# Kernel optimization log

Hardware: AMD Instinct MI355X
Metric: run time of the kernel (lower is better)

The kernel has to match this reference:

```python
import jax, jax.numpy as jnp
import numpy as np

SCORE_THRESHOLD = 0.15
IOU_THRESHOLD = 0.5
MAX_OUTPUT = 10          # tf.image.non_max_suppression(..., 10, ...)
NUM_CLASSES = 80
NUM_ANCHORS = 5
NEG = -1e9               # score for suppressed / below-threshold boxes


def setup_inputs() -> dict:
    key = jax.random.key(0)
    k1, k2 = jax.random.split(key)
    preds = jax.random.normal(k1, (16, 52, 52, NUM_ANCHORS * (5 + NUM_CLASSES)), dtype=jnp.float32)
    # anchor priors in grid-cell units, typical YOLOv2 range
    anchors = jax.random.uniform(k2, (NUM_ANCHORS, 2), dtype=jnp.float32, minval=0.5, maxval=6.0)
    return {"preds": preds, "anchors": anchors}


def _decode(preds, anchors):
    """YOLOv2 head decode (the `_interpret_prediction` callable)."""
    B, H, W, _ = preds.shape
    A = anchors.shape[0]
    p = preds.reshape(B, H, W, A, 5 + NUM_CLASSES)
    gy, gx = jnp.meshgrid(jnp.arange(H, dtype=preds.dtype),
                          jnp.arange(W, dtype=preds.dtype), indexing="ij")
    grid = jnp.stack([gx, gy], axis=-1)[None, :, :, None, :]   # (1,H,W,1,2) in (x,y)
    dims = jnp.array([W, H], dtype=preds.dtype)
    box_xy = (jax.nn.sigmoid(p[..., :2]) + grid) / dims        # normalized centers
    box_wh = jnp.exp(p[..., 2:4]) * anchors[None, None, None, :, :] / dims
    box_confidence = jax.nn.sigmoid(p[..., 4:5])
    box_class_probs = jax.nn.softmax(p[..., 5:], axis=-1)
    return box_xy, box_wh, box_confidence, box_class_probs


def _iou(box, boxes):
    """IoU of one box (ymin,xmin,ymax,xmax) against all boxes [N,4]."""
    tl = jnp.maximum(box[:2], boxes[:, :2])
    br = jnp.minimum(box[2:], boxes[:, 2:])
    inter = jnp.prod(jnp.maximum(br - tl, 0.0), axis=-1)
    area1 = jnp.prod(jnp.maximum(box[2:] - box[:2], 0.0))
    area2 = jnp.prod(jnp.maximum(boxes[:, 2:] - boxes[:, :2], 0.0), axis=-1)
    return inter / (area1 + area2 - inter + 1e-9)


def reference(preds, anchors):
    box_xy, box_wh, box_confidence, box_class_probs = _decode(preds, anchors)
    box_mins = box_xy - box_wh / 2.0
    box_maxes = box_xy + box_wh / 2.0
    # (ymin, xmin, ymax, xmax), matching the K.concatenate in the source
    boxes = jnp.concatenate([box_mins[..., 1:2], box_mins[..., 0:1],
                             box_maxes[..., 1:2], box_maxes[..., 0:1]], axis=-1)
    box_scores = box_confidence * box_class_probs
    box_classes = jnp.argmax(box_scores, axis=-1)
    box_class_scores = jnp.max(box_scores, axis=-1)

    boxes = boxes.reshape(-1, 4)                       # [N,4]
    scores = box_class_scores.reshape(-1)              # [N]
    classes = box_classes.reshape(-1).astype(preds.dtype)

    # score-threshold mask: instead of boolean_mask (dynamic shape), kill scores
    live = jnp.where(scores >= SCORE_THRESHOLD, scores, NEG)

    # greedy NMS, fixed MAX_OUTPUT iterations (semantics of tf.image.non_max_suppression)
    def step(cur_scores, _):
        i = jnp.argmax(cur_scores)
        s = cur_scores[i]
        valid = s > NEG / 2
        box = boxes[i]
        ious = _iou(box, boxes)
        nxt = jnp.where(ious > IOU_THRESHOLD, NEG, cur_scores).at[i].set(NEG)
        row = jnp.where(valid,
                        jnp.concatenate([box, s[None], classes[i][None]]),
                        jnp.zeros((6,), dtype=preds.dtype))
        return nxt, row

    _, rows = jax.lax.scan(step, live, None, length=MAX_OUTPUT)
    return rows  # [10, 6] = (ymin, xmin, ymax, xmax, score, class); zero rows = padding
```

## Files before the change

### kernel.cpp

```cpp
#include <hip/hip_runtime.h>
#include <math.h>

#define A_N      5
#define GRID_HW  52
#define NCLS     80
#define CH       85
#define SCORE_T  0.15f
#define IOU_T    0.5f
#define NEGV     (-1e9f)
#define MAXOUT   10

#define BPB          64
#define DEC_THREADS  256
#define TILE_FLOATS  (BPB * CH)
#define TILE_F4      (TILE_FLOATS / 4)

#define NMS_THREADS  1024
#define NMS_LBOX     8192
#define KA           (NMS_LBOX / NMS_THREADS)

__global__ __launch_bounds__(DEC_THREADS) void decode_kernel(
    const float* __restrict__ preds,
    const float* __restrict__ anchors,
    float4* __restrict__ pbox, float* __restrict__ pscore,
    float* __restrict__ pcls,
    int* __restrict__ counter, int N, int capacity)
{
    __shared__ __align__(16) float lds[TILE_FLOATS];

    const int tile = blockIdx.x;
    const long long tile_f4_base = (long long)tile * TILE_F4;
    const long long total_f4 = ((long long)N * CH) / 4;
    const float4* src = (const float4*)preds;
    float4* dst = (float4*)lds;

#pragma unroll
    for (int k = 0; k < (TILE_F4 + DEC_THREADS - 1) / DEC_THREADS; ++k) {
        int idx = (int)threadIdx.x + k * DEC_THREADS;
        if (idx < TILE_F4 && (tile_f4_base + idx) < total_f4)
            dst[idx] = src[tile_f4_base + idx];
    }
    __syncthreads();

    const int b = (int)threadIdx.x >> 2;
    const int q = (int)threadIdx.x & 3;
    const int gi = tile * BPB + b;
    const float* bp = lds + b * CH;
    const float* cl = bp + 5 + q * 20;

    float m = cl[0];
    int   am = q * 20;
#pragma unroll
    for (int j = 1; j < 20; ++j) {
        float x = cl[j];
        if (x > m) { m = x; am = q * 20 + j; }
    }
    float s = 0.0f;
#pragma unroll
    for (int j = 0; j < 20; ++j) s += expf(cl[j] - m);

#pragma unroll
    for (int off = 1; off <= 2; off <<= 1) {
        float m2 = __shfl_xor(m, off);
        float s2 = __shfl_xor(s, off);
        int   am2 = __shfl_xor(am, off);
        float M = fmaxf(m, m2);
        s = s * expf(m - M) + s2 * expf(m2 - M);
        if (m2 > m || (m2 == m && am2 < am)) am = am2;
        m = M;
    }

    if (q == 0 && gi < N) {
        float conf  = 1.0f / (1.0f + expf(-bp[4]));
        float score = conf / s;
        if (score >= SCORE_T) {
            int a = gi % A_N;
            int t = gi / A_N;
            int w = t % GRID_HW;
            int h = (t / GRID_HW) % GRID_HW;
            const float inv = 1.0f / (float)GRID_HW;
            float cx = (1.0f / (1.0f + expf(-bp[0])) + (float)w) * inv;
            float cy = (1.0f / (1.0f + expf(-bp[1])) + (float)h) * inv;
            float bw = expf(bp[2]) * anchors[2 * a]     * inv;
            float bh = expf(bp[3]) * anchors[2 * a + 1] * inv;

            int pos = atomicAdd(counter, 1);
            if (pos < capacity) {
                pbox[pos]   = make_float4(cy - 0.5f * bh, cx - 0.5f * bw,
                                          cy + 0.5f * bh, cx + 0.5f * bw);
                pscore[pos] = score;
                pcls[pos]   = (float)am;
            }
        }
    }
}

__global__ __launch_bounds__(NMS_THREADS) void nms_kernel(
    const float4* __restrict__ pbox, float* __restrict__ pscore,
    const float* __restrict__ pcls, const int* __restrict__ counter,
    int capacity, float* __restrict__ out)
{
    __shared__ __align__(16) float4 lbox[NMS_LBOX];
    __shared__ float psc[16];
    __shared__ int   pix[16];
    __shared__ int   swi;

    int M = *counter;
    if (M > capacity) M = capacity;
    const int tid  = (int)threadIdx.x;
    const int lane = tid & 63;
    const int wid  = tid >> 6;

    if (M <= NMS_LBOX) {
        float sc[KA];
#pragma unroll
        for (int k = 0; k < KA; ++k) {
            int j = tid + (k << 10);
            sc[k] = (j < M) ? pscore[j] : -INFINITY;
            if (j < M) lbox[j] = pbox[j];
        }
        __syncthreads();

        for (int it = 0; it < MAXOUT; ++it) {
            float bs = -INFINITY; int bi = -1;
#pragma unroll
            for (int k = 0; k < KA; ++k) {
                if (sc[k] > bs) { bs = sc[k]; bi = tid + (k << 10); }
            }
#pragma unroll
            for (int off = 32; off; off >>= 1) {
                float os = __shfl_xor(bs, off);
                int   oi = __shfl_xor(bi, off);
                if (os > bs || (os == bs && oi != -1 && (bi == -1 || oi < bi))) {
                    bs = os; bi = oi;
                }
            }
            if (lane == 0) { psc[wid] = bs; pix[wid] = bi; }
            __syncthreads();

            if (wid == 0 && lane < 16) {
                bs = psc[lane]; bi = pix[lane];
#pragma unroll
                for (int off = 8; off; off >>= 1) {
                    float os = __shfl_xor(bs, off);
                    int   oi = __shfl_xor(bi, off);
                    if (os > bs || (os == bs && oi != -1 && (bi == -1 || oi < bi))) {
                        bs = os; bi = oi;
                    }
                }
                if (lane == 0) {
                    bool valid = (bi >= 0) && (bs > NEGV * 0.5f);
                    swi = valid ? bi : -1;
                    if (valid) {
                        float4 b = lbox[bi];
                        out[it*6+0] = b.x; out[it*6+1] = b.y;
                        out[it*6+2] = b.z; out[it*6+3] = b.w;
                        out[it*6+4] = bs;  out[it*6+5] = pcls[bi];
                    } else {
                        out[it*6+0] = 0.f; out[it*6+1] = 0.f; out[it*6+2] = 0.f;
                        out[it*6+3] = 0.f; out[it*6+4] = 0.f; out[it*6+5] = 0.f;
                    }
                }
            }
            __syncthreads();

            int wi = swi;
            if (wi >= 0) {
                float4 wb = lbox[wi];
                float a1 = fmaxf(wb.z - wb.x, 0.f) * fmaxf(wb.w - wb.y, 0.f);
#pragma unroll
                for (int k = 0; k < KA; ++k) {
                    int j = tid + (k << 10);
                    if (j == wi) sc[k] = NEGV;
                    if (j < M) {
                        float4 bj = lbox[j];
                        float ty = fmaxf(wb.x, bj.x);
                        float tx = fmaxf(wb.y, bj.y);
                        float by = fminf(wb.z, bj.z);
                        float bx = fminf(wb.w, bj.w);
                        float inter = fmaxf(by - ty, 0.f) * fmaxf(bx - tx, 0.f);
                        float a2 = fmaxf(bj.z - bj.x, 0.f) * fmaxf(bj.w - bj.y, 0.f);
                        float iou = inter / (a1 + a2 - inter + 1e-9f);
                        if (iou > IOU_T) sc[k] = NEGV;
                    }
                }
            }
        }
    } else {
        for (int it = 0; it < MAXOUT; ++it) {
            float bs = -INFINITY; int bi = -1;
            for (int j = tid; j < M; j += NMS_THREADS) {
                float s = pscore[j];
                if (s > bs) { bs = s; bi = j; }
            }
#pragma unroll
            for (int off = 32; off; off >>= 1) {
                float os = __shfl_xor(bs, off);
                int   oi = __shfl_xor(bi, off);
                if (os > bs || (os == bs && oi != -1 && (bi == -1 || oi < bi))) {
                    bs = os; bi = oi;
                }
            }
            if (lane == 0) { psc[wid] = bs; pix[wid] = bi; }
            __syncthreads();
            if (wid == 0 && lane < 16) {
                bs = psc[lane]; bi = pix[lane];
#pragma unroll
                for (int off = 8; off; off >>= 1) {
                    float os = __shfl_xor(bs, off);
                    int   oi = __shfl_xor(bi, off);
                    if (os > bs || (os == bs && oi != -1 && (bi == -1 || oi < bi))) {
                        bs = os; bi = oi;
                    }
                }
                if (lane == 0) {
                    bool valid = (bi >= 0) && (bs > NEGV * 0.5f);
                    swi = valid ? bi : -1;
                    if (valid) {
                        float4 b = pbox[bi];
                        out[it*6+0] = b.x; out[it*6+1] = b.y;
                        out[it*6+2] = b.z; out[it*6+3] = b.w;
                        out[it*6+4] = bs;  out[it*6+5] = pcls[bi];
                        pscore[bi] = NEGV;
                    } else {
                        out[it*6+0] = 0.f; out[it*6+1] = 0.f; out[it*6+2] = 0.f;
                        out[it*6+3] = 0.f; out[it*6+4] = 0.f; out[it*6+5] = 0.f;
                    }
                }
            }
            __syncthreads();
            int wi = swi;
            if (wi >= 0) {
                float4 wb = pbox[wi];
                float a1 = fmaxf(wb.z - wb.x, 0.f) * fmaxf(wb.w - wb.y, 0.f);
                for (int j = tid; j < M; j += NMS_THREADS) {
                    float4 bj = pbox[j];
                    float ty = fmaxf(wb.x, bj.x);
                    float tx = fmaxf(wb.y, bj.y);
                    float by = fminf(wb.z, bj.z);
                    float bx = fminf(wb.w, bj.w);
                    float inter = fmaxf(by - ty, 0.f) * fmaxf(bx - tx, 0.f);
                    float a2 = fmaxf(bj.z - bj.x, 0.f) * fmaxf(bj.w - bj.y, 0.f);
                    float iou = inter / (a1 + a2 - inter + 1e-9f);
                    if (iou > IOU_T) pscore[j] = NEGV;
                }
            }
            __syncthreads();
        }
    }
}

extern "C" void kernel_launch(void* const* d_in, const int* in_sizes, int n_in,
                              void* d_out, int out_size, void* d_ws, size_t ws_size,
                              hipStream_t stream) {
    (void)n_in; (void)out_size;
    const float* preds   = (const float*)d_in[0];
    const float* anchors = (const float*)d_in[1];
    float* out = (float*)d_out;

    int N = in_sizes[0] / CH;

    char* ws = (char*)d_ws;
    int* counter = (int*)ws;
    size_t avail = (ws_size > 64) ? (ws_size - 64) : 0;
    long long cap = (long long)(avail / (sizeof(float4) + 2 * sizeof(float)));
    if (cap > N) cap = N;
    if (cap < 0) cap = 0;
    int capacity = (int)cap;

    float4* pbox  = (float4*)(ws + 64);
    float* pscore = (float*)(pbox + capacity);
    float* pcls   = pscore + capacity;

    hipMemsetAsync(counter, 0, sizeof(int), stream);

    int nTiles = (N + BPB - 1) / BPB;
    decode_kernel<<<nTiles, DEC_THREADS, 0, stream>>>(
        preds, anchors, pbox, pscore, pcls, counter, N, capacity);
    nms_kernel<<<1, NMS_THREADS, 0, stream>>>(
        pbox, pscore, pcls, counter, capacity, out);
}
```

Baseline: 66.89 us.

## Keep NMS candidate boxes in registers and use fast exp in decode

The NMS kernel no longer stages all candidate boxes in a 128 KB shared array. Each thread keeps its boxes in registers, and the winning box is broadcast through a small shared slot. A barrier is added at the end of each iteration to protect that slot. The decode kernel caches each thread's 20 class logits in registers and swaps expf for the faster, less accurate __expf intrinsic. Register pressure rises with 8 float4 plus 8 scores per thread at 1024 threads, which may cause spills.

```diff
diff --git a/kernel.cpp b/kernel.cpp
--- a/kernel.cpp
+++ b/kernel.cpp
@@ -16,8 +16,10 @@
 #define TILE_F4      (TILE_FLOATS / 4)
 
 #define NMS_THREADS  1024
-#define NMS_LBOX     8192
-#define KA           (NMS_LBOX / NMS_THREADS)
+#define NMS_RCAP     8192
+#define KA           (NMS_RCAP / NMS_THREADS)
+
+__device__ __forceinline__ float fexp(float x) { return __expf(x); }
 
 __global__ __launch_bounds__(DEC_THREADS) void decode_kernel(
     const float* __restrict__ preds,
@@ -48,16 +50,19 @@
     const float* bp = lds + b * CH;
     const float* cl = bp + 5 + q * 20;
 
-    float m = cl[0];
+    float r[20];
+#pragma unroll
+    for (int j = 0; j < 20; ++j) r[j] = cl[j];
+
+    float m = r[0];
     int   am = q * 20;
 #pragma unroll
     for (int j = 1; j < 20; ++j) {
-        float x = cl[j];
-        if (x > m) { m = x; am = q * 20 + j; }
+        if (r[j] > m) { m = r[j]; am = q * 20 + j; }
     }
     float s = 0.0f;
 #pragma unroll
-    for (int j = 0; j < 20; ++j) s += expf(cl[j] - m);
+    for (int j = 0; j < 20; ++j) s += fexp(r[j] - m);
 
 #pragma unroll
     for (int off = 1; off <= 2; off <<= 1) {
@@ -65,13 +70,13 @@
         float s2 = __shfl_xor(s, off);
         int   am2 = __shfl_xor(am, off);
         float M = fmaxf(m, m2);
-        s = s * expf(m - M) + s2 * expf(m2 - M);
+        s = s * fexp(m - M) + s2 * fexp(m2 - M);
         if (m2 > m || (m2 == m && am2 < am)) am = am2;
         m = M;
     }
 
     if (q == 0 && gi < N) {
-        float conf  = 1.0f / (1.0f + expf(-bp[4]));
+        float conf  = 1.0f / (1.0f + fexp(-bp[4]));
         float score = conf / s;
         if (score >= SCORE_T) {
             int a = gi % A_N;
@@ -79,10 +84,10 @@
             int w = t % GRID_HW;
             int h = (t / GRID_HW) % GRID_HW;
             const float inv = 1.0f / (float)GRID_HW;
-            float cx = (1.0f / (1.0f + expf(-bp[0])) + (float)w) * inv;
-            float cy = (1.0f / (1.0f + expf(-bp[1])) + (float)h) * inv;
-            float bw = expf(bp[2]) * anchors[2 * a]     * inv;
-            float bh = expf(bp[3]) * anchors[2 * a + 1] * inv;
+            float cx = (1.0f / (1.0f + fexp(-bp[0])) + (float)w) * inv;
+            float cy = (1.0f / (1.0f + fexp(-bp[1])) + (float)h) * inv;
+            float bw = fexp(bp[2]) * anchors[2 * a]     * inv;
+            float bh = fexp(bp[3]) * anchors[2 * a + 1] * inv;
 
             int pos = atomicAdd(counter, 1);
             if (pos < capacity) {
@@ -100,10 +105,10 @@
     const float* __restrict__ pcls, const int* __restrict__ counter,
     int capacity, float* __restrict__ out)
 {
-    __shared__ __align__(16) float4 lbox[NMS_LBOX];
     __shared__ float psc[16];
     __shared__ int   pix[16];
     __shared__ int   swi;
+    __shared__ float swb[4];
 
     int M = *counter;
     if (M > capacity) M = capacity;
@@ -111,15 +116,15 @@
     const int lane = tid & 63;
     const int wid  = tid >> 6;
 
-    if (M <= NMS_LBOX) {
-        float sc[KA];
+    if (M <= NMS_RCAP) {
+        float4 rb[KA];
+        float  sc[KA];
 #pragma unroll
         for (int k = 0; k < KA; ++k) {
             int j = tid + (k << 10);
-            sc[k] = (j < M) ? pscore[j] : -INFINITY;
-            if (j < M) lbox[j] = pbox[j];
-        }
-        __syncthreads();
+            if (j < M) { sc[k] = pscore[j]; rb[k] = pbox[j]; }
+            else       { sc[k] = -INFINITY; rb[k] = make_float4(0.f,0.f,0.f,0.f); }
+        }
 
         for (int it = 0; it < MAXOUT; ++it) {
             float bs = -INFINITY; int bi = -1;
@@ -152,7 +157,8 @@
                     bool valid = (bi >= 0) && (bs > NEGV * 0.5f);
                     swi = valid ? bi : -1;
                     if (valid) {
-                        float4 b = lbox[bi];
+                        float4 b = pbox[bi];
+                        swb[0] = b.x; swb[1] = b.y; swb[2] = b.z; swb[3] = b.w;
                         out[it*6+0] = b.x; out[it*6+1] = b.y;
                         out[it*6+2] = b.z; out[it*6+3] = b.w;
                         out[it*6+4] = bs;  out[it*6+5] = pcls[bi];
@@ -166,25 +172,23 @@
 
             int wi = swi;
             if (wi >= 0) {
-                float4 wb = lbox[wi];
-                float a1 = fmaxf(wb.z - wb.x, 0.f) * fmaxf(wb.w - wb.y, 0.f);
+                float wy0 = swb[0], wx0 = swb[1], wy1 = swb[2], wx1 = swb[3];
+                float a1 = fmaxf(wy1 - wy0, 0.f) * fmaxf(wx1 - wx0, 0.f);
 #pragma unroll
                 for (int k = 0; k < KA; ++k) {
                     int j = tid + (k << 10);
                     if (j == wi) sc[k] = NEGV;
-                    if (j < M) {
-                        float4 bj = lbox[j];
-                        float ty = fmaxf(wb.x, bj.x);
-                        float tx = fmaxf(wb.y, bj.y);
-                        float by = fminf(wb.z, bj.z);
-                        float bx = fminf(wb.w, bj.w);
-                        float inter = fmaxf(by - ty, 0.f) * fmaxf(bx - tx, 0.f);
-                        float a2 = fmaxf(bj.z - bj.x, 0.f) * fmaxf(bj.w - bj.y, 0.f);
-                        float iou = inter / (a1 + a2 - inter + 1e-9f);
-                        if (iou > IOU_T) sc[k] = NEGV;
-                    }
-                }
-            }
+                    float ty = fmaxf(wy0, rb[k].x);
+                    float tx = fmaxf(wx0, rb[k].y);
+                    float by = fminf(wy1, rb[k].z);
+                    float bx = fminf(wx1, rb[k].w);
+                    float inter = fmaxf(by - ty, 0.f) * fmaxf(bx - tx, 0.f);
+                    float a2 = fmaxf(rb[k].z - rb[k].x, 0.f) * fmaxf(rb[k].w - rb[k].y, 0.f);
+                    float iou = inter / (a1 + a2 - inter + 1e-9f);
+                    if (iou > IOU_T) sc[k] = NEGV;
+                }
+            }
+            __syncthreads();
         }
     } else {
         for (int it = 0; it < MAXOUT; ++it) {
@@ -218,6 +222,7 @@
                     swi = valid ? bi : -1;
                     if (valid) {
                         float4 b = pbox[bi];
+                        swb[0] = b.x; swb[1] = b.y; swb[2] = b.z; swb[3] = b.w;
                         out[it*6+0] = b.x; out[it*6+1] = b.y;
                         out[it*6+2] = b.z; out[it*6+3] = b.w;
                         out[it*6+4] = bs;  out[it*6+5] = pcls[bi];
@@ -231,14 +236,14 @@
             __syncthreads();
             int wi = swi;
             if (wi >= 0) {
-                float4 wb = pbox[wi];
-                float a1 = fmaxf(wb.z - wb.x, 0.f) * fmaxf(wb.w - wb.y, 0.f);
+                float wy0 = swb[0], wx0 = swb[1], wy1 = swb[2], wx1 = swb[3];
+                float a1 = fmaxf(wy1 - wy0, 0.f) * fmaxf(wx1 - wx0, 0.f);
                 for (int j = tid; j < M; j += NMS_THREADS) {
                     float4 bj = pbox[j];
-                    float ty = fmaxf(wb.x, bj.x);
-                    float tx = fmaxf(wb.y, bj.y);
-                    float by = fminf(wb.z, bj.z);
-                    float bx = fminf(wb.w, bj.w);
+                    float ty = fmaxf(wy0, bj.x);
+                    float tx = fmaxf(wx0, bj.y);
+                    float by = fminf(wy1, bj.z);
+                    float bx = fminf(wx1, bj.w);
                     float inter = fmaxf(by - ty, 0.f) * fmaxf(bx - tx, 0.f);
                     float a2 = fmaxf(bj.z - bj.x, 0.f) * fmaxf(bj.w - bj.y, 0.f);
                     float iou = inter / (a1 + a2 - inter + 1e-9f);
```

Result: slower. 76.88 us (+14.9%).
